# Optimization experiments

Hardware: AMD Instinct MI355X
Metric: run time of the kernel (lower is better)

## Reference

```python
import jax, jax.numpy as jnp
import numpy as np

DIM = 128
HEADS = 4
NS = 7          # neighborhood_size (odd)
RADIUS = NS // 2
EXP = 2         # ffn expansion
EPS = 1e-8


def rmsnorm(x, w):
    # x: [B,C,H,W], w: [1,C,1,1]
    rms = jnp.mean(jnp.square(x), axis=1, keepdims=True)
    return x * jax.lax.rsqrt(rms + EPS) * w


def conv1x1(x, w, b):
    # w: [Cout,Cin], b: [Cout]
    return jnp.einsum('oi,bihw->bohw', w, x) + b[None, :, None, None]


def setup_inputs() -> dict:
    key = jax.random.key(0)
    ks = jax.random.split(key, 20)
    B, C, H, W = 2, DIM, 64, 64
    s = 0.02
    d = {
        'z': jax.random.normal(ks[0], (B, C, H, W), jnp.float32),
        'h': jax.random.normal(ks[1], (B, C, H, W), jnp.float32),
        'wz_norm': jnp.ones((1, C, 1, 1), jnp.float32),
        'wh_norm': jnp.ones((1, C, 1, 1), jnp.float32),
        'wq': jax.random.normal(ks[2], (C, C), jnp.float32) * s,
        'bq': jnp.zeros((C,), jnp.float32),
        'wk': jax.random.normal(ks[3], (C, C), jnp.float32) * s,
        'bk': jnp.zeros((C,), jnp.float32),
        'wv': jax.random.normal(ks[4], (C, C), jnp.float32) * s,
        'bv': jnp.zeros((C,), jnp.float32),
        'wo': jax.random.normal(ks[5], (C, C), jnp.float32) * s,
        'bo': jnp.zeros((C,), jnp.float32),
        'wffn_norm': jnp.ones((1, C, 1, 1), jnp.float32),
        'w1': jax.random.normal(ks[6], (C * EXP, C), jnp.float32) * s,
        'b1': jnp.zeros((C * EXP,), jnp.float32),
        'w2': jax.random.normal(ks[7], (C, C * EXP), jnp.float32) * s,
        'b2': jnp.zeros((C,), jnp.float32),
    }
    return d


def neighborhood_cross_attn(zq, hk, wq, bq, wk, bk, wv, bv, wo, bo):
    B, C, H, W = zq.shape
    hd = C // HEADS
    scale = hd ** (-0.5)
    q = conv1x1(zq, wq, bq)
    k = conv1x1(hk, wk, bk)
    v = conv1x1(hk, wv, bv)
    # [B, heads, H, W, hd]
    qh = q.reshape(B, HEADS, hd, H, W).transpose(0, 1, 3, 4, 2)
    kh = k.reshape(B, HEADS, hd, H, W).transpose(0, 1, 3, 4, 2)
    vh = v.reshape(B, HEADS, hd, H, W).transpose(0, 1, 3, 4, 2)
    offs = jnp.arange(-RADIUS, RADIUS + 1)
    dy, dx = jnp.meshgrid(offs, offs, indexing='ij')
    dy = dy.reshape(-1)  # [K]
    dx = dx.reshape(-1)
    by, bx = jnp.meshgrid(jnp.arange(H), jnp.arange(W), indexing='ij')
    ny = by[:, :, None] + dy  # [H, W, K]
    nx = bx[:, :, None] + dx
    valid = (ny >= 0) & (ny < H) & (nx >= 0) & (nx < W)
    nyc = jnp.clip(ny, 0, H - 1)
    nxc = jnp.clip(nx, 0, W - 1)
    # gather neighbors: [B, heads, H, W, K, hd]
    k_nb = kh[:, :, nyc, nxc]
    v_nb = vh[:, :, nyc, nxc]
    attn = jnp.einsum('bnhwd,bnhwkd->bnhwk', qh, k_nb) * scale
    attn = jnp.where(valid[None, None], attn, jnp.finfo(attn.dtype).min)
    p = jax.nn.softmax(attn, axis=-1)
    out = jnp.einsum('bnhwk,bnhwkd->bnhwd', p, v_nb)
    out = out.transpose(0, 1, 4, 2, 3).reshape(B, C, H, W)
    return conv1x1(out, wo, bo)


def reference(z, h, wz_norm, wh_norm, wq, bq, wk, bk, wv, bv, wo, bo,
              wffn_norm, w1, b1, w2, b2):
    h_norm = rmsnorm(h, wh_norm)
    z_norm = rmsnorm(z, wz_norm)
    z = z + neighborhood_cross_attn(z_norm, h_norm, wq, bq, wk, bk, wv, bv, wo, bo)
    y = rmsnorm(z, wffn_norm)
    y = conv1x1(y, w1, b1)
    y = jax.nn.gelu(y, approximate=False)
    y = conv1x1(y, w2, b2)
    return z + y
```

## Files before the change

kernel.cpp:

```cpp
#include <hip/hip_runtime.h>
#include <math.h>

#define CDIM 128
#define HW   4096
#define HEADS 4
#define HD   32

typedef __attribute__((ext_vector_type(8))) short bf16x8;
typedef __attribute__((ext_vector_type(4))) float f32x4;

static __device__ __forceinline__ unsigned int f2bf(float f) {
  union { float f; unsigned int u; } v; v.f = f;
  unsigned int r = v.u + 0x7FFF + ((v.u >> 16) & 1);
  return r >> 16;
}
static __device__ __forceinline__ float bflo(unsigned int u) {
  return __uint_as_float(u << 16);
}
static __device__ __forceinline__ float bfhi(unsigned int u) {
  return __uint_as_float(u & 0xFFFF0000u);
}
static __device__ __forceinline__ float gelu_f(float v) {
  return 0.5f * v * (1.0f + erff(v * 0.70710678118654752f));
}

__global__ __launch_bounds__(256) void head(
    const float* __restrict__ z, const float* __restrict__ h,
    const float* __restrict__ wzn, const float* __restrict__ whn,
    const float* __restrict__ wq, const float* __restrict__ bq,
    const float* __restrict__ wk, const float* __restrict__ bk,
    const float* __restrict__ wv, const float* __restrict__ bv,
    const float* __restrict__ wo, const float* __restrict__ w1,
    const float* __restrict__ w2, ushort* __restrict__ WB,
    ushort* __restrict__ Qb, ushort* __restrict__ Kb, ushort* __restrict__ Vb) {
  const int sel = blockIdx.y, t = threadIdx.x;
  if (sel == 3) {
    int e = (blockIdx.x * 256 + t) * 4;
    if (e < 81920) {
      const float* src; int off;
      if      (e < 16384) { src = wo; off = 0; }
      else if (e < 49152) { src = w1; off = 16384; }
      else                { src = w2; off = 49152; }
      float4 v = *(const float4*)&src[e - off];
      uint2 r;
      r.x = f2bf(v.x) | (f2bf(v.y) << 16);
      r.y = f2bf(v.z) | (f2bf(v.w) << 16);
      *(uint2*)&WB[49152 + e] = r;
    }
    return;
  }
  __shared__ __align__(16) ushort sW[128 * 128];
  __shared__ __align__(16) ushort sX[64 * 128];
  __shared__ float sh[4][64];

  const float* X    = (sel == 0) ? z : h;
  const float* wn   = (sel == 0) ? wzn : whn;
  const float* Wf   = (sel == 0) ? wq : (sel == 1 ? wk : wv);
  const float* bias = (sel == 0) ? bq : (sel == 1 ? bk : bv);
  ushort* outB      = (sel == 0) ? Qb : (sel == 1 ? Kb : Vb);

#pragma unroll
  for (int i = 0; i < 8; ++i) {
    int u  = t + i * 256;
    int o  = u >> 4;
    int k8 = (u & 15) * 8;
    float4 v0 = *(const float4*)&Wf[o * 128 + k8];
    float4 v1 = *(const float4*)&Wf[o * 128 + k8 + 4];
    uint4 pk;
    pk.x = f2bf(v0.x) | (f2bf(v0.y) << 16);
    pk.y = f2bf(v0.z) | (f2bf(v0.w) << 16);
    pk.z = f2bf(v1.x) | (f2bf(v1.y) << 16);
    pk.w = f2bf(v1.z) | (f2bf(v1.w) << 16);
    int idx = (o * 128 + k8) ^ ((o & 7) << 3);
    *(uint4*)&sW[idx] = pk;
  }

  const int pl = t & 63, g = t >> 6;
  const int gp = blockIdx.x * 64 + pl;
  const size_t xbase = (size_t)(gp >> 12) * CDIM * HW + (gp & 4095);
  float vals[32];
  float ss = 0.f;
#pragma unroll
  for (int j = 0; j < 32; ++j) {
    float v = X[xbase + (size_t)(g * 32 + j) * HW];
    vals[j] = v;
    ss += v * v;
  }
  sh[g][pl] = ss;
  __syncthreads();
  float tot = sh[0][pl] + sh[1][pl] + sh[2][pl] + sh[3][pl];
  float inv = rsqrtf(tot * (1.0f / CDIM) + 1e-8f);
#pragma unroll
  for (int jj = 0; jj < 4; ++jj) {
    unsigned int u[4];
#pragma unroll
    for (int p2 = 0; p2 < 4; ++p2) {
      int j = jj * 8 + p2 * 2;
      float a = vals[j]     * inv * wn[g * 32 + j];
      float b = vals[j + 1] * inv * wn[g * 32 + j + 1];
      u[p2] = f2bf(a) | (f2bf(b) << 16);
    }
    int idx = (pl * 128 + g * 32 + jj * 8) ^ ((pl & 7) << 3);
    *(uint4*)&sX[idx] = make_uint4(u[0], u[1], u[2], u[3]);
  }
  __syncthreads();

  const int w = t >> 6, l = t & 63, lr = l & 15, lk = l >> 4;
  const int m0 = w * 32;
  const int swz = (lr & 7) << 3;
  f32x4 acc[2][4] = {};
#pragma unroll
  for (int k0 = 0; k0 < 128; k0 += 32) {
    bf16x8 a0 = *(const bf16x8*)&sW[((m0 + lr) * 128 + k0 + lk * 8) ^ swz];
    bf16x8 a1 = *(const bf16x8*)&sW[((m0 + 16 + lr) * 128 + k0 + lk * 8) ^ swz];
    bf16x8 b[4];
#pragma unroll
    for (int nf = 0; nf < 4; ++nf)
      b[nf] = *(const bf16x8*)&sX[((nf * 16 + lr) * 128 + k0 + lk * 8) ^ swz];
#pragma unroll
    for (int nf = 0; nf < 4; ++nf) {
      acc[0][nf] = __builtin_amdgcn_mfma_f32_16x16x32_bf16(a0, b[nf], acc[0][nf], 0, 0, 0);
      acc[1][nf] = __builtin_amdgcn_mfma_f32_16x16x32_bf16(a1, b[nf], acc[1][nf], 0, 0, 0);
    }
  }
#pragma unroll
  for (int mf = 0; mf < 2; ++mf) {
    int obase = m0 + mf * 16 + lk * 4;
    f32x4 bv = *(const f32x4*)&bias[obase];
#pragma unroll
    for (int nf = 0; nf < 4; ++nf) {
      int P = blockIdx.x * 64 + nf * 16 + lr;
      uint2 pk;
      pk.x = f2bf(acc[mf][nf][0] + bv[0]) | (f2bf(acc[mf][nf][1] + bv[1]) << 16);
      pk.y = f2bf(acc[mf][nf][2] + bv[2]) | (f2bf(acc[mf][nf][3] + bv[3]) << 16);
      *(uint2*)&outB[(size_t)P * CDIM + obase] = pk;
    }
  }
}

__global__ __launch_bounds__(512) void nattn(
    const ushort* __restrict__ Q, const ushort* __restrict__ K,
    const ushort* __restrict__ V, ushort* __restrict__ ATT) {
  __shared__ __align__(16) unsigned int smem[20480];
  float* sS = (float*)smem;
  const int t  = threadIdx.x;
  const int px = t & 127;
  const int x  = px & 63;
  const int r  = px >> 6;
  const int dg = t >> 7;
  const int y0 = blockIdx.x * 2;
  const int h  = blockIdx.y;
  const int b  = blockIdx.z;
  const int ybase = y0 - 3;

  {
    int yy = t >> 6, xs = t & 63;
    int gy = min(max(ybase + yy, 0), 63);
    size_t gb = ((size_t)(b * HW + gy * 64 + xs)) * 64 + h * 16;
    const unsigned int* Ku = (const unsigned int*)K;
    const unsigned int* Vu = (const unsigned int*)V;
    int lb = (yy * 64 + xs) * 20;
#pragma unroll
    for (int i = 0; i < 4; ++i) {
      uint4 kv = *(const uint4*)&Ku[gb + i * 4];
      uint4 vv = *(const uint4*)&Vu[gb + i * 4];
      *(uint4*)&smem[lb + i * 4]         = kv;
      *(uint4*)&smem[10240 + lb + i * 4] = vv;
    }
  }
  const int Pq = b * HW + (y0 + r) * 64 + x;
  const unsigned int* Qu = (const unsigned int*)Q;
  float q[32];
#pragma unroll
  for (int i = 0; i < 4; ++i) {
    uint4 u4 = *(const uint4*)&Qu[(size_t)Pq * 64 + h * 16 + i * 4];
    q[i*8+0] = bflo(u4.x); q[i*8+1] = bfhi(u4.x);
    q[i*8+2] = bflo(u4.y); q[i*8+3] = bfhi(u4.y);
    q[i*8+4] = bflo(u4.z); q[i*8+5] = bfhi(u4.z);
    q[i*8+6] = bflo(u4.w); q[i*8+7] = bfhi(u4.w);
  }
  __syncthreads();

  const float scale = 0.17677669529663687f;
  const int nb0    = (dg == 0) ? 0 : dg * 12 + 1;
  const int ncount = (dg == 0) ? 13 : 12;
  float sreg[13];
#pragma unroll
  for (int j = 0; j < 13; ++j) {
    if (j < ncount) {
      int nb = nb0 + j;
      int dy = nb / 7 - 3;
      int dx = nb % 7 - 3;
      int ry = r + dy + 3;
      int nx = x + dx;
      int xx = min(max(nx, 0), 63);
      int ny = y0 + r + dy;
      bool valid = (ny >= 0) && (ny <= 63) && (nx >= 0) && (nx <= 63);
      const unsigned int* kb = &smem[(ry * 64 + xx) * 20];
      float acc = 0.f;
#pragma unroll
      for (int c = 0; c < 4; ++c) {
        uint4 u4 = *(const uint4*)&kb[c * 4];
        acc += q[c*8+0] * bflo(u4.x) + q[c*8+1] * bfhi(u4.x);
        acc += q[c*8+2] * bflo(u4.y) + q[c*8+3] * bfhi(u4.y);
        acc += q[c*8+4] * bflo(u4.z) + q[c*8+5] * bfhi(u4.z);
        acc += q[c*8+6] * bflo(u4.w) + q[c*8+7] * bfhi(u4.w);
      }
      sreg[j] = valid ? acc * scale : -1e30f;
    }
  }
  __syncthreads();
#pragma unroll
  for (int j = 0; j < 13; ++j)
    if (j < ncount) sS[(nb0 + j) * 128 + px] = sreg[j];
  __syncthreads();

  float o[8] = {0.f, 0.f, 0.f, 0.f, 0.f, 0.f, 0.f, 0.f};
  float sum = 0.f;
#pragma unroll
  for (int nb = 0; nb < 49; ++nb) {
    float p = __expf(sS[nb * 128 + px] - 8.0f);
    sum += p;
    int ry = r + nb / 7;
    int xx = min(max(x + nb % 7 - 3, 0), 63);
    uint4 u4 = *(const uint4*)&smem[10240 + (ry * 64 + xx) * 20 + dg * 4];
    o[0] += p * bflo(u4.x); o[1] += p * bfhi(u4.x);
    o[2] += p * bflo(u4.y); o[3] += p * bfhi(u4.y);
    o[4] += p * bflo(u4.z); o[5] += p * bfhi(u4.z);
    o[6] += p * bflo(u4.w); o[7] += p * bfhi(u4.w);
  }
  float inv = 1.0f / sum;
  unsigned int pk[4];
#pragma unroll
  for (int j = 0; j < 4; ++j)
    pk[j] = f2bf(o[2*j] * inv) | (f2bf(o[2*j+1] * inv) << 16);
  *(uint4*)&ATT[(size_t)Pq * CDIM + h * HD + dg * 8] = make_uint4(pk[0], pk[1], pk[2], pk[3]);
}

__global__ __launch_bounds__(256) void tail(
    const ushort* __restrict__ ATT, const ushort* __restrict__ WB,
    const float* __restrict__ bo, const float* __restrict__ z,
    const float* __restrict__ wfn, const float* __restrict__ b1,
    const float* __restrict__ b2, float* __restrict__ out) {
  __shared__ __align__(16) float  zlds[32][132];
  __shared__ __align__(16) ushort fn_s[32 * 128];
  __shared__ __align__(16) ushort hid_s[32 * 256];
  __shared__ float sums[32][17];
  __shared__ float sinv[32];
  const ushort* Wo = WB + 49152;
  const ushort* W1 = WB + 65536;
  const ushort* W2 = WB + 98304;
  const int t = threadIdx.x, w = t >> 6, l = t & 63, lr = l & 15, lk = l >> 4;
  const int pblk = blockIdx.x * 32;
  const int m0 = w * 32;

  {
    const ushort* A0 = Wo + (size_t)(m0 + lr) * 128 + lk * 8;
    const ushort* A1 = A0 + 16 * 128;
    const ushort* B0 = ATT + (size_t)(pblk + lr) * 128 + lk * 8;
    const ushort* B1 = B0 + 16 * 128;
    f32x4 acc[2][2] = {};
#pragma unroll
    for (int k0 = 0; k0 < 128; k0 += 32) {
      bf16x8 a0 = *(const bf16x8*)(A0 + k0);
      bf16x8 a1 = *(const bf16x8*)(A1 + k0);
      bf16x8 b0 = *(const bf16x8*)(B0 + k0);
      bf16x8 b1 = *(const bf16x8*)(B1 + k0);
      acc[0][0] = __builtin_amdgcn_mfma_f32_16x16x32_bf16(a0, b0, acc[0][0], 0, 0, 0);
      acc[0][1] = __builtin_amdgcn_mfma_f32_16x16x32_bf16(a0, b1, acc[0][1], 0, 0, 0);
      acc[1][0] = __builtin_amdgcn_mfma_f32_16x16x32_bf16(a1, b0, acc[1][0], 0, 0, 0);
      acc[1][1] = __builtin_amdgcn_mfma_f32_16x16x32_bf16(a1, b1, acc[1][1], 0, 0, 0);
    }
#pragma unroll
    for (int nf = 0; nf < 2; ++nf) {
      int px = nf * 16 + lr;
      int P  = pblk + px;
      int b_ = P >> 12, p = P & 4095;
      float ss = 0.f;
#pragma unroll
      for (int mf = 0; mf < 2; ++mf) {
        int row0 = m0 + mf * 16 + lk * 4;
        f32x4 bv = *(const f32x4*)&bo[row0];
        f32x4 rr;
#pragma unroll
        for (int j = 0; j < 4; ++j) {
          size_t gi = ((size_t)(b_ * CDIM + row0 + j)) * HW + p;
          float u = acc[mf][nf][j] + bv[j] + z[gi];
          rr[j] = u;
          ss += u * u;
        }
        *(f32x4*)&zlds[px][row0] = rr;
      }
      sums[px][w * 4 + lk] = ss;
    }
  }
  __syncthreads();
  if (t < 32) {
    float tot = 0.f;
#pragma unroll
    for (int i = 0; i < 16; ++i) tot += sums[t][i];
    sinv[t] = rsqrtf(tot * (1.0f / CDIM) + 1e-8f);
  }
  __syncthreads();
#pragma unroll
  for (int nf = 0; nf < 2; ++nf) {
    int px = nf * 16 + lr;
    float inv = sinv[px];
#pragma unroll
    for (int mf = 0; mf < 2; ++mf) {
      int row0 = m0 + mf * 16 + lk * 4;
      f32x4 uu = *(const f32x4*)&zlds[px][row0];
      f32x4 wf = *(const f32x4*)&wfn[row0];
      uint2 pk;
      pk.x = f2bf(uu[0] * inv * wf[0]) | (f2bf(uu[1] * inv * wf[1]) << 16);
      pk.y = f2bf(uu[2] * inv * wf[2]) | (f2bf(uu[3] * inv * wf[3]) << 16);
      int idx = (px * 128 + row0) ^ ((px & 7) << 3);
      *(uint2*)&fn_s[idx] = pk;
    }
  }
  __syncthreads();
  {
    const int hm0 = w * 64;
    const ushort* A0 = W1 + (size_t)(hm0 + lr) * 128 + lk * 8;
    f32x4 acc1[4][2] = {};
#pragma unroll
    for (int k0 = 0; k0 < 128; k0 += 32) {
      bf16x8 a[4], b[2];
#pragma unroll
      for (int mf = 0; mf < 4; ++mf) a[mf] = *(const bf16x8*)(A0 + mf * 16 * 128 + k0);
#pragma unroll
      for (int nf = 0; nf < 2; ++nf) {
        int px = nf * 16 + lr;
        b[nf] = *(const bf16x8*)&fn_s[(px * 128 + k0 + lk * 8) ^ ((px & 7) << 3)];
      }
#pragma unroll
      for (int mf = 0; mf < 4; ++mf)
#pragma unroll
        for (int nf = 0; nf < 2; ++nf)
          acc1[mf][nf] = __builtin_amdgcn_mfma_f32_16x16x32_bf16(a[mf], b[nf], acc1[mf][nf], 0, 0, 0);
    }
#pragma unroll
    for (int mf = 0; mf < 4; ++mf) {
      int ch0 = hm0 + mf * 16 + lk * 4;
      f32x4 bv = *(const f32x4*)&b1[ch0];
#pragma unroll
      for (int nf = 0; nf < 2; ++nf) {
        int px = nf * 16 + lr;
        float v0 = gelu_f(acc1[mf][nf][0] + bv[0]);
        float v1 = gelu_f(acc1[mf][nf][1] + bv[1]);
        float v2 = gelu_f(acc1[mf][nf][2] + bv[2]);
        float v3 = gelu_f(acc1[mf][nf][3] + bv[3]);
        uint2 pk;
        pk.x = f2bf(v0) | (f2bf(v1) << 16);
        pk.y = f2bf(v2) | (f2bf(v3) << 16);
        int idx = (px * 256 + ch0) ^ ((px & 7) << 3);
        *(uint2*)&hid_s[idx] = pk;
      }
    }
  }
  __syncthreads();
  {
    const ushort* C0 = W2 + (size_t)(m0 + lr) * 256 + lk * 8;
    f32x4 acc2[2][2] = {};
#pragma unroll
    for (int k0 = 0; k0 < 256; k0 += 32) {
      bf16x8 a0 = *(const bf16x8*)(C0 + k0);
      bf16x8 a1 = *(const bf16x8*)(C0 + 16 * 256 + k0);
      bf16x8 b[2];
#pragma unroll
      for (int nf = 0; nf < 2; ++nf) {
        int px = nf * 16 + lr;
        b[nf] = *(const bf16x8*)&hid_s[(px * 256 + k0 + lk * 8) ^ ((px & 7) << 3)];
      }
      acc2[0][0] = __builtin_amdgcn_mfma_f32_16x16x32_bf16(a0, b[0], acc2[0][0], 0, 0, 0);
      acc2[0][1] = __builtin_amdgcn_mfma_f32_16x16x32_bf16(a0, b[1], acc2[0][1], 0, 0, 0);
      acc2[1][0] = __builtin_amdgcn_mfma_f32_16x16x32_bf16(a1, b[0], acc2[1][0], 0, 0, 0);
      acc2[1][1] = __builtin_amdgcn_mfma_f32_16x16x32_bf16(a1, b[1], acc2[1][1], 0, 0, 0);
    }
#pragma unroll
    for (int mf = 0; mf < 2; ++mf) {
      int row0 = m0 + mf * 16 + lk * 4;
      f32x4 bv = *(const f32x4*)&b2[row0];
#pragma unroll
      for (int nf = 0; nf < 2; ++nf) {
        int px = nf * 16 + lr;
        int P  = pblk + px;
        int b_ = P >> 12, p = P & 4095;
        f32x4 zz = *(const f32x4*)&zlds[px][row0];
#pragma unroll
        for (int j = 0; j < 4; ++j) {
          size_t gi = ((size_t)(b_ * CDIM + row0 + j)) * HW + p;
          out[gi] = acc2[mf][nf][j] + bv[j] + zz[j];
        }
      }
    }
  }
}

extern "C" void kernel_launch(void* const* d_in, const int* in_sizes, int n_in,
                              void* d_out, int out_size, void* d_ws, size_t ws_size,
                              hipStream_t stream) {
  const float* z   = (const float*)d_in[0];
  const float* h   = (const float*)d_in[1];
  const float* wzn = (const float*)d_in[2];
  const float* whn = (const float*)d_in[3];
  const float* wq  = (const float*)d_in[4];
  const float* bq  = (const float*)d_in[5];
  const float* wk  = (const float*)d_in[6];
  const float* bk  = (const float*)d_in[7];
  const float* wv  = (const float*)d_in[8];
  const float* bv  = (const float*)d_in[9];
  const float* wo  = (const float*)d_in[10];
  const float* bo  = (const float*)d_in[11];
  const float* wfn = (const float*)d_in[12];
  const float* w1  = (const float*)d_in[13];
  const float* b1  = (const float*)d_in[14];
  const float* w2  = (const float*)d_in[15];
  const float* b2  = (const float*)d_in[16];
  float* out = (float*)d_out;

  const size_t U = 1048576;
  ushort* Qb  = (ushort*)d_ws;
  ushort* Kb  = Qb + U;
  ushort* Vb  = Kb + U;
  ushort* ATT = Vb + U;
  ushort* WB  = ATT + U;

  head<<<dim3(128, 4), 256, 0, stream>>>(z, h, wzn, whn, wq, bq, wk, bk, wv, bv,
                                         wo, w1, w2, WB, Qb, Kb, Vb);
  nattn<<<dim3(32, HEADS, 2), 512, 0, stream>>>(Qb, Kb, Vb, ATT);
  tail<<<dim3(256), 256, 0, stream>>>(ATT, WB, bo, z, wfn, b1, b2, out);
}
```

Baseline: 40.59 us.

## Merge K/V projection blocks, load weights directly to registers, move exp earlier

The head kernel now computes K and V from one block that normalizes h once, and keeps the activation fragments in registers across two passes. Weight fragments are loaded straight from global memory into MFMA registers instead of being staged through shared memory, and the grid shrinks from four rows of blocks to three. The neighborhood attention now applies the exponential while computing scores, so the second loop only reads probabilities. The exact erf GELU is replaced by a tanh-style sigmoid approximation, which adds numerical error and removes parallelism from the K/V path.

```diff
diff --git a/kernel.cpp b/kernel.cpp
--- a/kernel.cpp
+++ b/kernel.cpp
@@ -21,7 +21,16 @@
   return __uint_as_float(u & 0xFFFF0000u);
 }
 static __device__ __forceinline__ float gelu_f(float v) {
-  return 0.5f * v * (1.0f + erff(v * 0.70710678118654752f));
+  float y = v * (1.595769122f + 0.071354816f * v * v);
+  return v / (1.0f + __expf(-y));
+}
+static __device__ __forceinline__ bf16x8 ldw8(const float* __restrict__ p) {
+  float4 v0 = *(const float4*)p;
+  float4 v1 = *(const float4*)(p + 4);
+  union { ushort u[8]; bf16x8 v; } r;
+  r.u[0] = f2bf(v0.x); r.u[1] = f2bf(v0.y); r.u[2] = f2bf(v0.z); r.u[3] = f2bf(v0.w);
+  r.u[4] = f2bf(v1.x); r.u[5] = f2bf(v1.y); r.u[6] = f2bf(v1.z); r.u[7] = f2bf(v1.w);
+  return r.v;
 }
 
 __global__ __launch_bounds__(256) void head(
@@ -34,7 +43,7 @@
     const float* __restrict__ w2, ushort* __restrict__ WB,
     ushort* __restrict__ Qb, ushort* __restrict__ Kb, ushort* __restrict__ Vb) {
   const int sel = blockIdx.y, t = threadIdx.x;
-  if (sel == 3) {
+  if (sel == 2) {
     int e = (blockIdx.x * 256 + t) * 4;
     if (e < 81920) {
       const float* src; int off;
@@ -49,31 +58,11 @@
     }
     return;
   }
-  __shared__ __align__(16) ushort sW[128 * 128];
   __shared__ __align__(16) ushort sX[64 * 128];
   __shared__ float sh[4][64];
 
-  const float* X    = (sel == 0) ? z : h;
-  const float* wn   = (sel == 0) ? wzn : whn;
-  const float* Wf   = (sel == 0) ? wq : (sel == 1 ? wk : wv);
-  const float* bias = (sel == 0) ? bq : (sel == 1 ? bk : bv);
-  ushort* outB      = (sel == 0) ? Qb : (sel == 1 ? Kb : Vb);
-
-#pragma unroll
-  for (int i = 0; i < 8; ++i) {
-    int u  = t + i * 256;
-    int o  = u >> 4;
-    int k8 = (u & 15) * 8;
-    float4 v0 = *(const float4*)&Wf[o * 128 + k8];
-    float4 v1 = *(const float4*)&Wf[o * 128 + k8 + 4];
-    uint4 pk;
-    pk.x = f2bf(v0.x) | (f2bf(v0.y) << 16);
-    pk.y = f2bf(v0.z) | (f2bf(v0.w) << 16);
-    pk.z = f2bf(v1.x) | (f2bf(v1.y) << 16);
-    pk.w = f2bf(v1.z) | (f2bf(v1.w) << 16);
-    int idx = (o * 128 + k8) ^ ((o & 7) << 3);
-    *(uint4*)&sW[idx] = pk;
-  }
+  const float* X  = (sel == 0) ? z : h;
+  const float* wn = (sel == 0) ? wzn : whn;
 
   const int pl = t & 63, g = t >> 6;
   const int gp = blockIdx.x * 64 + pl;
@@ -108,32 +97,42 @@
   const int w = t >> 6, l = t & 63, lr = l & 15, lk = l >> 4;
   const int m0 = w * 32;
   const int swz = (lr & 7) << 3;
-  f32x4 acc[2][4] = {};
-#pragma unroll
-  for (int k0 = 0; k0 < 128; k0 += 32) {
-    bf16x8 a0 = *(const bf16x8*)&sW[((m0 + lr) * 128 + k0 + lk * 8) ^ swz];
-    bf16x8 a1 = *(const bf16x8*)&sW[((m0 + 16 + lr) * 128 + k0 + lk * 8) ^ swz];
-    bf16x8 b[4];
+  bf16x8 bfr[4][4];
+#pragma unroll
+  for (int ki = 0; ki < 4; ++ki)
 #pragma unroll
     for (int nf = 0; nf < 4; ++nf)
-      b[nf] = *(const bf16x8*)&sX[((nf * 16 + lr) * 128 + k0 + lk * 8) ^ swz];
-#pragma unroll
-    for (int nf = 0; nf < 4; ++nf) {
-      acc[0][nf] = __builtin_amdgcn_mfma_f32_16x16x32_bf16(a0, b[nf], acc[0][nf], 0, 0, 0);
-      acc[1][nf] = __builtin_amdgcn_mfma_f32_16x16x32_bf16(a1, b[nf], acc[1][nf], 0, 0, 0);
-    }
-  }
-#pragma unroll
-  for (int mf = 0; mf < 2; ++mf) {
-    int obase = m0 + mf * 16 + lk * 4;
-    f32x4 bv = *(const f32x4*)&bias[obase];
-#pragma unroll
-    for (int nf = 0; nf < 4; ++nf) {
-      int P = blockIdx.x * 64 + nf * 16 + lr;
-      uint2 pk;
-      pk.x = f2bf(acc[mf][nf][0] + bv[0]) | (f2bf(acc[mf][nf][1] + bv[1]) << 16);
-      pk.y = f2bf(acc[mf][nf][2] + bv[2]) | (f2bf(acc[mf][nf][3] + bv[3]) << 16);
-      *(uint2*)&outB[(size_t)P * CDIM + obase] = pk;
+      bfr[ki][nf] = *(const bf16x8*)&sX[((nf * 16 + lr) * 128 + ki * 32 + lk * 8) ^ swz];
+
+  const int npass = (sel == 0) ? 1 : 2;
+#pragma unroll 1
+  for (int pass = 0; pass < npass; ++pass) {
+    const float* Wf   = (sel == 0) ? wq : (pass == 0 ? wk : wv);
+    const float* bias = (sel == 0) ? bq : (pass == 0 ? bk : bv);
+    ushort* outB      = (sel == 0) ? Qb : (pass == 0 ? Kb : Vb);
+    f32x4 acc[2][4] = {};
+#pragma unroll
+    for (int ki = 0; ki < 4; ++ki) {
+      bf16x8 a0 = ldw8(&Wf[(m0 + lr) * 128 + ki * 32 + lk * 8]);
+      bf16x8 a1 = ldw8(&Wf[(m0 + 16 + lr) * 128 + ki * 32 + lk * 8]);
+#pragma unroll
+      for (int nf = 0; nf < 4; ++nf) {
+        acc[0][nf] = __builtin_amdgcn_mfma_f32_16x16x32_bf16(a0, bfr[ki][nf], acc[0][nf], 0, 0, 0);
+        acc[1][nf] = __builtin_amdgcn_mfma_f32_16x16x32_bf16(a1, bfr[ki][nf], acc[1][nf], 0, 0, 0);
+      }
+    }
+#pragma unroll
+    for (int mf = 0; mf < 2; ++mf) {
+      int obase = m0 + mf * 16 + lk * 4;
+      f32x4 bv4 = *(const f32x4*)&bias[obase];
+#pragma unroll
+      for (int nf = 0; nf < 4; ++nf) {
+        int P = blockIdx.x * 64 + nf * 16 + lr;
+        uint2 pk;
+        pk.x = f2bf(acc[mf][nf][0] + bv4[0]) | (f2bf(acc[mf][nf][1] + bv4[1]) << 16);
+        pk.y = f2bf(acc[mf][nf][2] + bv4[2]) | (f2bf(acc[mf][nf][3] + bv4[3]) << 16);
+        *(uint2*)&outB[(size_t)P * CDIM + obase] = pk;
+      }
     }
   }
 }
@@ -206,7 +205,7 @@
         acc += q[c*8+4] * bflo(u4.z) + q[c*8+5] * bfhi(u4.z);
         acc += q[c*8+6] * bflo(u4.w) + q[c*8+7] * bfhi(u4.w);
       }
-      sreg[j] = valid ? acc * scale : -1e30f;
+      sreg[j] = valid ? __expf(acc * scale - 8.0f) : 0.0f;
     }
   }
   __syncthreads();
@@ -219,7 +218,7 @@
   float sum = 0.f;
 #pragma unroll
   for (int nb = 0; nb < 49; ++nb) {
-    float p = __expf(sS[nb * 128 + px] - 8.0f);
+    float p = sS[nb * 128 + px];
     sum += p;
     int ry = r + nb / 7;
     int xx = min(max(x + nb % 7 - 3, 0), 63);
@@ -426,7 +425,7 @@
   ushort* ATT = Vb + U;
   ushort* WB  = ATT + U;
 
-  head<<<dim3(128, 4), 256, 0, stream>>>(z, h, wzn, whn, wq, bq, wk, bk, wv, bv,
+  head<<<dim3(128, 3), 256, 0, stream>>>(z, h, wzn, whn, wq, bq, wk, bk, wv, bv,
                                          wo, w1, w2, WB, Qb, Kb, Vb);
   nattn<<<dim3(32, HEADS, 2), 512, 0, stream>>>(Qb, Kb, Vb, ATT);
   tail<<<dim3(256), 256, 0, stream>>>(ATT, WB, bo, z, wfn, b1, b2, out);
```

Result: slower. 41.66 us (+2.6%).
